# Optimization experiments

Measured on AMD Instinct MI355X. Metric: run time of the kernel, lower is better.

## Reference

```python
import jax, jax.numpy as jnp
import numpy as np
from jax import lax

# init kwargs (hardcoded per module config)
T_D = 0.3            # condensation radius
T_B = 0.85           # min beta threshold
FEATURE_LENGTH = 9   # x[:, FEATURE_LENGTH:] are predictions
N_TOT_FEAT = 17      # => n_ccoords = 17 - 14 = 3
MAX_COND = 1024      # static pad size for the boolean-mask gather output

B = 4
S = 250000
N = B * S


def setup_inputs() -> dict:
    key = jax.random.key(0)
    kx, = jax.random.split(key, 1)
    x = jax.random.uniform(kx, (N, N_TOT_FEAT), dtype=jnp.float32)  # betas in [0,1)
    row_splits = jnp.arange(B + 1, dtype=jnp.int32) * S             # equal ragged splits
    return {"x": x, "row_splits": row_splits}


def _condense(x, n_seg, seg_len):
    """Greedy BuildCondensates (hard/soft=False): per segment, repeatedly pick the
    unassigned point of max beta (>= T_B), assign all unassigned points within
    radius T_D of it in cluster-coordinate space, until no candidate remains."""
    n_ccoords = x.shape[-1] - 14
    x_pred = x[:, FEATURE_LENGTH:]
    betas = x_pred[:, 0].reshape(n_seg, seg_len)                     # (B,S)
    cc = x_pred[:, x_pred.shape[-1] - n_ccoords:].reshape(n_seg, seg_len, n_ccoords)
    col = jnp.arange(seg_len, dtype=jnp.int32)[None, :]              # (1,S)

    asso0 = -jnp.ones((n_seg, seg_len), jnp.int32)
    iscond0 = jnp.zeros((n_seg, seg_len), jnp.int32)

    def body(state):
        asso, iscond, _ = state
        unassigned = asso < 0
        score = jnp.where(unassigned, betas, -jnp.inf)
        max_idx = jnp.argmax(score, axis=1).astype(jnp.int32)        # (B,) per-segment argmax beta
        max_beta = jnp.take_along_axis(score, max_idx[:, None], axis=1)[:, 0]
        found = max_beta >= T_B                                      # (B,)
        c = jnp.take_along_axis(cc, max_idx[:, None, None], axis=1)  # (B,1,nc)
        distsq = jnp.sum((cc - c) ** 2, axis=-1)                     # (B,S)
        assign = unassigned & (distsq < T_D * T_D) & found[:, None]
        asso = jnp.where(assign, max_idx[:, None], asso)
        iscond = jnp.where(assign & (col == max_idx[:, None]), 1, iscond)
        return (asso, iscond, jnp.any(found))

    asso, iscond, _ = lax.while_loop(lambda s: s[2], body,
                                     (asso0, iscond0, jnp.array(True)))
    ncond_per_seg = jnp.sum(iscond, axis=1, dtype=jnp.int32)         # (B,)
    # output row splits for condensates: [0, cumsum...]
    ncond = jnp.concatenate([jnp.zeros((1,), jnp.int32),
                             jnp.cumsum(ncond_per_seg).astype(jnp.int32)])
    return asso, iscond.reshape(-1), ncond


def reference(x, row_splits):
    n_seg = row_splits.shape[0] - 1          # static
    seg_len = x.shape[0] // n_seg            # equal splits assumed (matches setup)
    _, iscond, ncond = _condense(x, n_seg, seg_len)
    # boolean-mask gather dout = x[iscond > 0], padded to static MAX_COND rows
    idx = jnp.nonzero(iscond > 0, size=MAX_COND, fill_value=0)[0]
    total = jnp.sum(iscond)
    valid = (jnp.arange(MAX_COND) < total).astype(x.dtype)           # (K,)
    dout = x[idx] * valid[:, None]                                   # (K, F), zero-padded
    return dout, ncond
```

## Files before the change

kernel.cpp:

```cpp
#include <hip/hip_runtime.h>
#include <stdint.h>

typedef unsigned long long u64;
typedef unsigned int u32;
typedef unsigned char u8;


#define DSQ(ax,ay,az,bx,by,bz) \
    __fadd_rn(__fadd_rn(__fmul_rn(__fsub_rn(ax,bx),__fsub_rn(ax,bx)), \
                        __fmul_rn(__fsub_rn(ay,by),__fsub_rn(ay,by))), \
              __fmul_rn(__fsub_rn(az,bz),__fsub_rn(az,bz)))

#define INS5(k, cx, cy, cz) do { u64 _k = (k); \
    if (_k > K5) { \
      if (_k > K4) { K5 = K4; \
        if (_k > K3) { K4 = K3; X4=X3; Y4=Y3; Z4=Z3; \
          if (_k > K2) { K3 = K2; X3=X2; Y3=Y2; Z3=Z2; \
            if (_k > K1) { K2 = K1; X2=X1; Y2=Y1; Z2=Z1; \
                           K1 = _k; X1=(cx); Y1=(cy); Z1=(cz); } \
            else { K2 = _k; X2=(cx); Y2=(cy); Z2=(cz); } } \
          else { K3 = _k; X3=(cx); Y3=(cy); Z3=(cz); } } \
        else { K4 = _k; X4=(cx); Y4=(cy); Z4=(cz); } } \
      else K5 = _k; \
    } } while (0)

__launch_bounds__(256)
__global__ void filter_scan0(const float* __restrict__ x, int Sg, int chunkG, int bps,
                             int* __restrict__ segCount,
                             float4* __restrict__ A, int* __restrict__ iA,
                             u8* __restrict__ aliveB, int CAP,
                             u64* __restrict__ btK, float4* __restrict__ btC) {
    __shared__ float4 stg[1024];
    __shared__ int sgi[1024];
    __shared__ int s_cnt, s_base;
    __shared__ u64 mK[4][5];
    __shared__ float mC[4][12];
    const int b = blockIdx.x;
    const int s = b / bps, c = b % bps;
    const int tid = threadIdx.x, lane = tid & 63, wid = tid >> 6;
    const int segG0 = s * Sg;
    const int g = segG0 + c * chunkG + tid;
    const bool valid = (g < segG0 + Sg) && (tid < chunkG);
    if (tid == 0) s_cnt = 0;
    __syncthreads();

    float be0=0, be1=0, be2=0, be3=0;
    float4 cc0, cc1, cc2, cc3;
    int r0 = 0;
    if (valid) {
        const float4* p = (const float4*)x + (size_t)g * 17;
        float4 v2 = p[2],  v3 = p[3],  v4 = p[4];
        float4 v6 = p[6],  v7 = p[7],  v8 = p[8];
        float4 v10 = p[10], v12 = p[12];
        float4 v15 = p[15], v16 = p[16];
        r0 = g * 4;
        be0 = v2.y;  cc0 = make_float4(v3.z,  v3.w,  v4.x,  be0);
        be1 = v6.z;  cc1 = make_float4(v7.w,  v8.x,  v8.y,  be1);
        be2 = v10.w; cc2 = make_float4(v12.x, v12.y, v12.z, be2);
        be3 = v15.x; cc3 = make_float4(v16.y, v16.z, v16.w, be3);
    }
    bool h0 = valid && (be0 >= 0.85f), h1 = valid && (be1 >= 0.85f);
    bool h2 = valid && (be2 >= 0.85f), h3 = valid && (be3 >= 0.85f);
    int nh = (h0?1:0) + (h1?1:0) + (h2?1:0) + (h3?1:0);
    int p0 = 0;
    if (nh) p0 = atomicAdd(&s_cnt, nh);
    if (h0) { if (p0 < 1024) { stg[p0] = cc0; sgi[p0] = r0;     } p0++; }
    if (h1) { if (p0 < 1024) { stg[p0] = cc1; sgi[p0] = r0 + 1; } p0++; }
    if (h2) { if (p0 < 1024) { stg[p0] = cc2; sgi[p0] = r0 + 2; } p0++; }
    if (h3) { if (p0 < 1024) { stg[p0] = cc3; sgi[p0] = r0 + 3; } p0++; }
    __syncthreads();
    if (tid == 0) s_base = atomicAdd(&segCount[s], min(s_cnt, 1024));
    __syncthreads();
    int cnt = min(s_cnt, 1024);

    u64 K1=0,K2=0,K3=0,K4=0,K5=0;
    float X1=0,Y1=0,Z1=0,X2=0,Y2=0,Z2=0,X3=0,Y3=0,Z3=0,X4=0,Y4=0,Z4=0;
    for (int k = tid; k < cnt; k += 256) {
        int pos = s_base + k;
        float4 cd = stg[k];
        int gi = sgi[k];
        if (pos < CAP) {
            A[(size_t)s * CAP + pos] = cd;
            iA[(size_t)s * CAP + pos] = gi;
            aliveB[(size_t)s * CAP + pos] = 1;
            u64 key = ((u64)__float_as_uint(cd.w) << 32) | (u64)(~(u32)gi);
            INS5(key, cd.x, cd.y, cd.z);
        }
    }
    for (int off = 32; off > 0; off >>= 1) {
        u64 o1=__shfl_xor(K1,off), o2=__shfl_xor(K2,off), o3=__shfl_xor(K3,off),
            o4=__shfl_xor(K4,off), o5=__shfl_xor(K5,off);
        float a1=__shfl_xor(X1,off), b1=__shfl_xor(Y1,off), c1=__shfl_xor(Z1,off);
        float a2=__shfl_xor(X2,off), b2=__shfl_xor(Y2,off), c2=__shfl_xor(Z2,off);
        float a3=__shfl_xor(X3,off), b3=__shfl_xor(Y3,off), c3=__shfl_xor(Z3,off);
        float a4=__shfl_xor(X4,off), b4=__shfl_xor(Y4,off), c4=__shfl_xor(Z4,off);
        INS5(o1,a1,b1,c1); INS5(o2,a2,b2,c2); INS5(o3,a3,b3,c3); INS5(o4,a4,b4,c4);
        if (o5 > K5) K5 = o5;
    }
    if (lane == 0) {
        mK[wid][0]=K1; mK[wid][1]=K2; mK[wid][2]=K3; mK[wid][3]=K4; mK[wid][4]=K5;
        mC[wid][0]=X1; mC[wid][1]=Y1; mC[wid][2]=Z1; mC[wid][3]=X2; mC[wid][4]=Y2;
        mC[wid][5]=Z2; mC[wid][6]=X3; mC[wid][7]=Y3; mC[wid][8]=Z3; mC[wid][9]=X4;
        mC[wid][10]=Y4; mC[wid][11]=Z4;
    }
    __syncthreads();
    if (tid == 0) {
        for (int w = 1; w < 4; ++w) {
            INS5(mK[w][0], mC[w][0], mC[w][1], mC[w][2]);
            INS5(mK[w][1], mC[w][3], mC[w][4], mC[w][5]);
            INS5(mK[w][2], mC[w][6], mC[w][7], mC[w][8]);
            INS5(mK[w][3], mC[w][9], mC[w][10], mC[w][11]);
            if (mK[w][4] > K5) K5 = mK[w][4];
        }
        btK[(size_t)b*5+0]=K1; btK[(size_t)b*5+1]=K2; btK[(size_t)b*5+2]=K3;
        btK[(size_t)b*5+3]=K4; btK[(size_t)b*5+4]=K5;
        btC[(size_t)b*4+0]=make_float4(X1,Y1,Z1,0.f);
        btC[(size_t)b*4+1]=make_float4(X2,Y2,Z2,0.f);
        btC[(size_t)b*4+2]=make_float4(X3,Y3,Z3,0.f);
        btC[(size_t)b*4+3]=make_float4(X4,Y4,Z4,0.f);
    }
}

__launch_bounds__(256)
__global__ void scan_r(const float4* __restrict__ A, const int* __restrict__ iA,
                       const int* __restrict__ segCount, int CAP,
                       const float4* __restrict__ gctr,
                       const int* __restrict__ condTotal, const int* __restrict__ scanned,
                       const int* __restrict__ doneF, u8* __restrict__ aliveB,
                       u64* __restrict__ btK, float4* __restrict__ btC,
                       int* __restrict__ aliveCnt) {
    const int b = blockIdx.x;
    const int s = b >> 8, c = b & 255;
    const int tid = threadIdx.x, lane = tid & 63, wid = tid >> 6;
    __shared__ float4 ctrL[1024];
    __shared__ u64 mK[4][5];
    __shared__ float mC[4][12];
    __shared__ int wAl[4];
    if (doneF[s]) return;

    int n = segCount[s]; if (n > CAP) n = CAP;
    const int c0 = scanned[s], c1 = condTotal[s];
    const int nc = c1 - c0;
    for (int i = tid; i < nc; i += 256) ctrL[i] = gctr[(size_t)s * 1024 + c0 + i];
    __syncthreads();

    const int chunkC = (n + 255) >> 8;
    const int j0 = c * chunkC;
    const int j1 = min(j0 + chunkC, n);

    u64 K1=0,K2=0,K3=0,K4=0,K5=0;
    float X1=0,Y1=0,Z1=0,X2=0,Y2=0,Z2=0,X3=0,Y3=0,Z3=0,X4=0,Y4=0,Z4=0;
    int myAlive = 0;
    for (int j = j0 + tid; j < j1; j += 256) {
        if (!aliveB[(size_t)s * CAP + j]) continue;
        float4 cd = A[(size_t)s * CAP + j];
        bool live = true;
        for (int m = 0; m < nc; ++m) {
            float4 q = ctrL[m];
            if (DSQ(cd.x, cd.y, cd.z, q.x, q.y, q.z) < 0.09f) { live = false; break; }
        }
        if (!live) { aliveB[(size_t)s * CAP + j] = 0; continue; }
        ++myAlive;
        u64 key = ((u64)__float_as_uint(cd.w) << 32) | (u64)(~(u32)iA[(size_t)s * CAP + j]);
        INS5(key, cd.x, cd.y, cd.z);
    }
    for (int off = 32; off > 0; off >>= 1) {
        u64 o1=__shfl_xor(K1,off), o2=__shfl_xor(K2,off), o3=__shfl_xor(K3,off),
            o4=__shfl_xor(K4,off), o5=__shfl_xor(K5,off);
        float a1=__shfl_xor(X1,off), b1=__shfl_xor(Y1,off), c1v=__shfl_xor(Z1,off);
        float a2=__shfl_xor(X2,off), b2=__shfl_xor(Y2,off), c2v=__shfl_xor(Z2,off);
        float a3=__shfl_xor(X3,off), b3=__shfl_xor(Y3,off), c3v=__shfl_xor(Z3,off);
        float a4=__shfl_xor(X4,off), b4=__shfl_xor(Y4,off), c4v=__shfl_xor(Z4,off);
        INS5(o1,a1,b1,c1v); INS5(o2,a2,b2,c2v); INS5(o3,a3,b3,c3v); INS5(o4,a4,b4,c4v);
        if (o5 > K5) K5 = o5;
        myAlive += __shfl_xor(myAlive, off);
    }
    if (lane == 0) {
        mK[wid][0]=K1; mK[wid][1]=K2; mK[wid][2]=K3; mK[wid][3]=K4; mK[wid][4]=K5;
        mC[wid][0]=X1; mC[wid][1]=Y1; mC[wid][2]=Z1; mC[wid][3]=X2; mC[wid][4]=Y2;
        mC[wid][5]=Z2; mC[wid][6]=X3; mC[wid][7]=Y3; mC[wid][8]=Z3; mC[wid][9]=X4;
        mC[wid][10]=Y4; mC[wid][11]=Z4;
        wAl[wid] = myAlive;
    }
    __syncthreads();
    if (tid == 0) {
        for (int w = 1; w < 4; ++w) {
            INS5(mK[w][0], mC[w][0], mC[w][1], mC[w][2]);
            INS5(mK[w][1], mC[w][3], mC[w][4], mC[w][5]);
            INS5(mK[w][2], mC[w][6], mC[w][7], mC[w][8]);
            INS5(mK[w][3], mC[w][9], mC[w][10], mC[w][11]);
            if (mK[w][4] > K5) K5 = mK[w][4];
        }
        btK[(size_t)b*5+0]=K1; btK[(size_t)b*5+1]=K2; btK[(size_t)b*5+2]=K3;
        btK[(size_t)b*5+3]=K4; btK[(size_t)b*5+4]=K5;
        btC[(size_t)b*4+0]=make_float4(X1,Y1,Z1,0.f);
        btC[(size_t)b*4+1]=make_float4(X2,Y2,Z2,0.f);
        btC[(size_t)b*4+2]=make_float4(X3,Y3,Z3,0.f);
        btC[(size_t)b*4+3]=make_float4(X4,Y4,Z4,0.f);
        int tot = wAl[0] + wAl[1] + wAl[2] + wAl[3];
        if (tot) atomicAdd(&aliveCnt[s], tot);
    }
}

__launch_bounds__(64)
__global__ void pop_k(const u64* __restrict__ btK, const float4* __restrict__ btC,
                      float4* __restrict__ gctr, int* __restrict__ gctrGi,
                      int* __restrict__ condTotal, int* __restrict__ scanned,
                      int* __restrict__ doneF, int* __restrict__ aliveCnt, int check) {
    const int s = blockIdx.x, lane = threadIdx.x;
    if (doneF[s]) return;
    if (check && aliveCnt[s] == 0) { if (lane == 0) doneF[s] = 1; return; }

    u64 k[16]; float4 c[16];
    u64 h = 0;
    #pragma unroll
    for (int q = 0; q < 16; ++q) {
        int bb = (s << 8) + (lane << 2) + (q >> 2);
        int slot = q & 3;
        k[q] = btK[(size_t)bb * 5 + slot];
        c[q] = btC[(size_t)bb * 4 + slot];
        if ((q & 3) == 0) {
            u64 k5 = btK[(size_t)bb * 5 + 4];
            if (k5 > h) h = k5;
        }
    }
    for (int off = 32; off > 0; off >>= 1) {
        u64 o = __shfl_xor(h, off);
        if (o > h) h = o;
    }
    const u64 H = h;

    int ct = condTotal[s];
    const int start = ct;
    while (ct < 1024) {
        u64 mk = k[0]; float4 mc = c[0];
        #pragma unroll
        for (int q = 1; q < 16; ++q)
            if (k[q] > mk) { mk = k[q]; mc = c[q]; }
        int src = lane;
        for (int off = 32; off > 0; off >>= 1) {
            u64 ok = __shfl_xor(mk, off);
            int os = __shfl_xor(src, off);
            if (ok > mk) { mk = ok; src = os; }
        }
        if (mk <= H) break;
        float cx = __shfl(mc.x, src);
        float cy = __shfl(mc.y, src);
        float cz = __shfl(mc.z, src);
        #pragma unroll
        for (int q = 0; q < 16; ++q)
            if (k[q] && DSQ(c[q].x, c[q].y, c[q].z, cx, cy, cz) < 0.09f) k[q] = 0;
        if (lane == 0) {
            gctr[(size_t)s * 1024 + ct] = make_float4(cx, cy, cz, 0.f);
            gctrGi[(size_t)s * 1024 + ct] = (int)(~(u32)(mk & 0xFFFFFFFFull));
        }
        ct++;
    }
    if (lane == 0) { scanned[s] = start; condTotal[s] = ct; aliveCnt[s] = 0; }
}

__launch_bounds__(1024)
__global__ void fallback_k(const float4* __restrict__ A, const int* __restrict__ iA,
                           const int* __restrict__ segCount, int CAP,
                           const float4* __restrict__ gctr, int* __restrict__ gctrGi,
                           int* __restrict__ condTotalG, int* __restrict__ scannedG,
                           const int* __restrict__ doneF, u8* __restrict__ aliveB) {
    const int s = blockIdx.x, tid = threadIdx.x, lane = tid & 63, wid = tid >> 6;
    __shared__ float4 ctr[1024];
    __shared__ int ctrGi[1024];
    __shared__ u64 wk[2][16];
    __shared__ float4 wc[2][16];
    __shared__ u64 s_H;
    __shared__ int s_alive;
    if (doneF[s]) return;

    const float4* cand = A + (size_t)s * CAP;
    const int* gia = iA + (size_t)s * CAP;
    u8* alv = aliveB + (size_t)s * CAP;
    int n = segCount[s]; if (n > CAP) n = CAP;
    int condTotal = condTotalG[s];
    int scanned = scannedG[s];
    for (int i = tid; i < condTotal; i += 1024) {
        ctr[i] = gctr[(size_t)s * 1024 + i];
        ctrGi[i] = gctrGi[(size_t)s * 1024 + i];
    }
    int passes = 0, par = 0;
    __syncthreads();

    while (true) {
        if (tid == 0) { s_H = 0; s_alive = 0; }
        __syncthreads();
        u64 k1 = 0, k2 = 0, k3 = 0;
        float4 C1 = make_float4(0,0,0,0), C2 = make_float4(0,0,0,0);
        int myAlive = 0;
        for (int j = tid; j < n; j += 1024) {
            if (!alv[j]) continue;
            float4 c = cand[j];
            bool live = true;
            for (int m = scanned; m < condTotal; ++m) {
                float4 q = ctr[m];
                if (DSQ(c.x, c.y, c.z, q.x, q.y, q.z) < 0.09f) { live = false; break; }
            }
            if (!live) { alv[j] = 0; continue; }
            ++myAlive;
            u64 key = ((u64)__float_as_uint(c.w) << 32) | (u64)(~(u32)gia[j]);
            if (key > k1)      { k3 = k2; k2 = k1; C2 = C1; k1 = key; C1 = c; }
            else if (key > k2) { k3 = k2; k2 = key; C2 = c; }
            else if (key > k3) { k3 = key; }
        }
        int asum = myAlive; u64 h = k3;
        for (int off = 32; off > 0; off >>= 1) {
            asum += __shfl_down(asum, off);
            u64 o = __shfl_down(h, off);
            if (o > h) h = o;
        }
        if (lane == 0) { atomicAdd(&s_alive, asum); atomicMax(&s_H, h); }
        __syncthreads();
        if (s_alive == 0) break;
        u64 H = s_H;
        scanned = condTotal;
        while (condTotal < 1024) {
            u64 mk; float4 bc;
            if (k1 >= k2) { mk = k1; bc = C1; } else { mk = k2; bc = C2; }
            for (int off = 32; off > 0; off >>= 1) {
                u64 ok = __shfl_xor(mk, off);
                float ox = __shfl_xor(bc.x, off);
                float oy = __shfl_xor(bc.y, off);
                float oz = __shfl_xor(bc.z, off);
                if (ok > mk) { mk = ok; bc.x = ox; bc.y = oy; bc.z = oz; }
            }
            if (lane == 0) { wk[par][wid] = mk; wc[par][wid] = bc; }
            __syncthreads();
            u64 bk = 0; int bL = 0;
            #pragma unroll
            for (int w = 0; w < 16; ++w) {
                u64 kk = wk[par][w];
                if (kk > bk) { bk = kk; bL = w; }
            }
            if (bk <= H) break;
            float4 cc = wc[par][bL];
            if (k1 && DSQ(C1.x, C1.y, C1.z, cc.x, cc.y, cc.z) < 0.09f) k1 = 0;
            if (k2 && DSQ(C2.x, C2.y, C2.z, cc.x, cc.y, cc.z) < 0.09f) k2 = 0;
            if (tid == 0) { ctr[condTotal] = cc; ctrGi[condTotal] = (int)(~(u32)(bk & 0xFFFFFFFFull)); }
            condTotal++;
            par ^= 1;
        }
        __syncthreads();
        if (condTotal >= 1024 || ++passes > 128) break;
    }

    for (int i = tid; i < condTotal; i += 1024)
        gctrGi[(size_t)s * 1024 + i] = ctrGi[i];
    if (tid == 0) condTotalG[s] = condTotal;
}

__global__ void finalize_kernel(const int* __restrict__ ctrGi,
                                const int* __restrict__ condTotal,
                                int* __restrict__ sorted, int* __restrict__ prefix,
                                float* __restrict__ ncond_out, int nseg, int rows) {
    __shared__ int lst[1024];
    __shared__ int pfx[9];
    int tid = threadIdx.x;
    if (tid == 0) {
        int acc = 0; pfx[0] = 0;
        for (int s2 = 0; s2 < nseg; s2++) { acc += condTotal[s2]; pfx[s2 + 1] = acc; }
    }
    __syncthreads();
    if (tid <= nseg) { prefix[tid] = pfx[tid]; ncond_out[tid] = (float)pfx[tid]; }
    for (int s2 = 0; s2 < nseg; s2++) {
        int ns = condTotal[s2]; if (ns > 1024) ns = 1024;
        for (int i = tid; i < ns; i += blockDim.x) lst[i] = ctrGi[(size_t)s2 * 1024 + i];
        __syncthreads();
        for (int i = tid; i < ns; i += blockDim.x) {
            int v = lst[i]; int rank = 0;
            for (int j = 0; j < ns; j++) rank += (lst[j] < v);
            int pos = pfx[s2] + rank;
            if (pos < rows) sorted[pos] = v;
        }
        __syncthreads();
    }
}

__global__ void emit_kernel(const float* __restrict__ x, const int* __restrict__ sorted,
                            const int* __restrict__ prefix, float* __restrict__ out,
                            int rows, int nseg) {
    int e = blockIdx.x * blockDim.x + threadIdx.x;
    if (e >= rows * 17) return;
    int total = prefix[nseg];
    int j = e / 17, k = e - j * 17;
    float v = 0.f;
    if (j < total) v = x[(size_t)sorted[j] * 17 + k];
    out[e] = v;
}

extern "C" void kernel_launch(void* const* d_in, const int* in_sizes, int n_in,
                              void* d_out, int out_size, void* d_ws, size_t ws_size,
                              hipStream_t stream) {
    const float* x = (const float*)d_in[0];
    const int nseg = in_sizes[1] - 1;
    const int N = in_sizes[0] / 17;
    const int S = N / nseg;
    const int rows = (out_size - (nseg + 1)) / 17;
    const int NROUNDS = 2;

    const int bps = 256;
    const int nBlocks = nseg * bps;
    const int Sg = S >> 2;
    const int chunkG = (Sg + bps - 1) / bps;

    size_t fixedBytes = (size_t)nseg * 1024 * 16  +
                        (size_t)nBlocks * 4 * 16  +
                        (size_t)nBlocks * 5 * 8   +
                        (size_t)nseg * 1024 * 4   +
                        (size_t)nseg * 4 * 5  +
                        (size_t)rows * 4 + (size_t)(nseg + 1) * 4 + 8192;
    size_t perCand = (size_t)nseg * (16 + 4 + 1);
    size_t avail = (ws_size > fixedBytes) ? (ws_size - fixedBytes) : 0;
    int CAP = (int)(avail / perCand);
    if (CAP > 65536) CAP = 65536;
    if (CAP < 1) CAP = 1;

    char* w = (char*)d_ws;
    float4* A    = (float4*)w;                 w += (size_t)nseg * CAP * 16;
    float4* ctr  = (float4*)w;                 w += (size_t)nseg * 1024 * 16;
    float4* btC  = (float4*)w;                 w += (size_t)nBlocks * 4 * 16;
    u64* btK     = (u64*)w;                    w += (size_t)nBlocks * 5 * 8;
    int* iA      = (int*)w;                    w += (size_t)nseg * CAP * 4;
    int* ctrGi   = (int*)w;                    w += (size_t)nseg * 1024 * 4;
    int* segCount  = (int*)w;                  w += (size_t)nseg * 4;
    int* condTotal = (int*)w;                  w += (size_t)nseg * 4;
    int* scanned   = (int*)w;                  w += (size_t)nseg * 4;
    int* doneF     = (int*)w;                  w += (size_t)nseg * 4;
    int* aliveCnt  = (int*)w;                  w += (size_t)nseg * 4;
    int* sorted    = (int*)w;                  w += (size_t)rows * 4;
    int* prefix    = (int*)w;                  w += (size_t)(nseg + 1) * 4;
    u8* aliveB     = (u8*)w;
    float* out = (float*)d_out;

    hipMemsetAsync(segCount, 0, (size_t)nseg * 5 * 4, stream);
    filter_scan0<<<nBlocks, 256, 0, stream>>>(x, Sg, chunkG, bps, segCount,
                                              A, iA, aliveB, CAP, btK, btC);
    pop_k<<<nseg, 64, 0, stream>>>(btK, btC, ctr, ctrGi, condTotal, scanned,
                                   doneF, aliveCnt, 0);
    for (int r = 0; r < NROUNDS; ++r) {
        scan_r<<<nBlocks, 256, 0, stream>>>(A, iA, segCount, CAP, ctr, condTotal,
                                            scanned, doneF, aliveB, btK, btC, aliveCnt);
        pop_k<<<nseg, 64, 0, stream>>>(btK, btC, ctr, ctrGi, condTotal, scanned,
                                       doneF, aliveCnt, 1);
    }
    fallback_k<<<nseg, 1024, 0, stream>>>(A, iA, segCount, CAP, ctr, ctrGi,
                                          condTotal, scanned, doneF, aliveB);
    finalize_kernel<<<1, 256, 0, stream>>>(ctrGi, condTotal, sorted, prefix,
                                           out + (size_t)rows * 17, nseg, rows);
    emit_kernel<<<(rows * 17 + 255) / 256, 256, 0, stream>>>(x, sorted, prefix, out,
                                                             rows, nseg);
}
```

Measured before the change: 158.0 us.

## Drop scan rounds, go straight to fallback, fuse finalize and emit

```diff
diff --git a/kernel.cpp b/kernel.cpp
--- a/kernel.cpp
+++ b/kernel.cpp
@@ -121,104 +121,22 @@
     }
 }
 
-__launch_bounds__(256)
-__global__ void scan_r(const float4* __restrict__ A, const int* __restrict__ iA,
-                       const int* __restrict__ segCount, int CAP,
-                       const float4* __restrict__ gctr,
-                       const int* __restrict__ condTotal, const int* __restrict__ scanned,
-                       const int* __restrict__ doneF, u8* __restrict__ aliveB,
-                       u64* __restrict__ btK, float4* __restrict__ btC,
-                       int* __restrict__ aliveCnt) {
-    const int b = blockIdx.x;
-    const int s = b >> 8, c = b & 255;
-    const int tid = threadIdx.x, lane = tid & 63, wid = tid >> 6;
-    __shared__ float4 ctrL[1024];
-    __shared__ u64 mK[4][5];
-    __shared__ float mC[4][12];
-    __shared__ int wAl[4];
-    if (doneF[s]) return;
-
-    int n = segCount[s]; if (n > CAP) n = CAP;
-    const int c0 = scanned[s], c1 = condTotal[s];
-    const int nc = c1 - c0;
-    for (int i = tid; i < nc; i += 256) ctrL[i] = gctr[(size_t)s * 1024 + c0 + i];
-    __syncthreads();
-
-    const int chunkC = (n + 255) >> 8;
-    const int j0 = c * chunkC;
-    const int j1 = min(j0 + chunkC, n);
-
-    u64 K1=0,K2=0,K3=0,K4=0,K5=0;
-    float X1=0,Y1=0,Z1=0,X2=0,Y2=0,Z2=0,X3=0,Y3=0,Z3=0,X4=0,Y4=0,Z4=0;
-    int myAlive = 0;
-    for (int j = j0 + tid; j < j1; j += 256) {
-        if (!aliveB[(size_t)s * CAP + j]) continue;
-        float4 cd = A[(size_t)s * CAP + j];
-        bool live = true;
-        for (int m = 0; m < nc; ++m) {
-            float4 q = ctrL[m];
-            if (DSQ(cd.x, cd.y, cd.z, q.x, q.y, q.z) < 0.09f) { live = false; break; }
-        }
-        if (!live) { aliveB[(size_t)s * CAP + j] = 0; continue; }
-        ++myAlive;
-        u64 key = ((u64)__float_as_uint(cd.w) << 32) | (u64)(~(u32)iA[(size_t)s * CAP + j]);
-        INS5(key, cd.x, cd.y, cd.z);
-    }
-    for (int off = 32; off > 0; off >>= 1) {
-        u64 o1=__shfl_xor(K1,off), o2=__shfl_xor(K2,off), o3=__shfl_xor(K3,off),
-            o4=__shfl_xor(K4,off), o5=__shfl_xor(K5,off);
-        float a1=__shfl_xor(X1,off), b1=__shfl_xor(Y1,off), c1v=__shfl_xor(Z1,off);
-        float a2=__shfl_xor(X2,off), b2=__shfl_xor(Y2,off), c2v=__shfl_xor(Z2,off);
-        float a3=__shfl_xor(X3,off), b3=__shfl_xor(Y3,off), c3v=__shfl_xor(Z3,off);
-        float a4=__shfl_xor(X4,off), b4=__shfl_xor(Y4,off), c4v=__shfl_xor(Z4,off);
-        INS5(o1,a1,b1,c1v); INS5(o2,a2,b2,c2v); INS5(o3,a3,b3,c3v); INS5(o4,a4,b4,c4v);
-        if (o5 > K5) K5 = o5;
-        myAlive += __shfl_xor(myAlive, off);
-    }
-    if (lane == 0) {
-        mK[wid][0]=K1; mK[wid][1]=K2; mK[wid][2]=K3; mK[wid][3]=K4; mK[wid][4]=K5;
-        mC[wid][0]=X1; mC[wid][1]=Y1; mC[wid][2]=Z1; mC[wid][3]=X2; mC[wid][4]=Y2;
-        mC[wid][5]=Z2; mC[wid][6]=X3; mC[wid][7]=Y3; mC[wid][8]=Z3; mC[wid][9]=X4;
-        mC[wid][10]=Y4; mC[wid][11]=Z4;
-        wAl[wid] = myAlive;
-    }
-    __syncthreads();
-    if (tid == 0) {
-        for (int w = 1; w < 4; ++w) {
-            INS5(mK[w][0], mC[w][0], mC[w][1], mC[w][2]);
-            INS5(mK[w][1], mC[w][3], mC[w][4], mC[w][5]);
-            INS5(mK[w][2], mC[w][6], mC[w][7], mC[w][8]);
-            INS5(mK[w][3], mC[w][9], mC[w][10], mC[w][11]);
-            if (mK[w][4] > K5) K5 = mK[w][4];
-        }
-        btK[(size_t)b*5+0]=K1; btK[(size_t)b*5+1]=K2; btK[(size_t)b*5+2]=K3;
-        btK[(size_t)b*5+3]=K4; btK[(size_t)b*5+4]=K5;
-        btC[(size_t)b*4+0]=make_float4(X1,Y1,Z1,0.f);
-        btC[(size_t)b*4+1]=make_float4(X2,Y2,Z2,0.f);
-        btC[(size_t)b*4+2]=make_float4(X3,Y3,Z3,0.f);
-        btC[(size_t)b*4+3]=make_float4(X4,Y4,Z4,0.f);
-        int tot = wAl[0] + wAl[1] + wAl[2] + wAl[3];
-        if (tot) atomicAdd(&aliveCnt[s], tot);
-    }
-}
-
 __launch_bounds__(64)
 __global__ void pop_k(const u64* __restrict__ btK, const float4* __restrict__ btC,
                       float4* __restrict__ gctr, int* __restrict__ gctrGi,
                       int* __restrict__ condTotal, int* __restrict__ scanned,
-                      int* __restrict__ doneF, int* __restrict__ aliveCnt, int check) {
+                      int* __restrict__ doneF, int* __restrict__ aliveCnt) {
     const int s = blockIdx.x, lane = threadIdx.x;
-    if (doneF[s]) return;
-    if (check && aliveCnt[s] == 0) { if (lane == 0) doneF[s] = 1; return; }
-
-    u64 k[16]; float4 c[16];
+
+    u64 k[16]; float cx16[16], cy16[16], cz16[16];
     u64 h = 0;
     #pragma unroll
     for (int q = 0; q < 16; ++q) {
         int bb = (s << 8) + (lane << 2) + (q >> 2);
         int slot = q & 3;
         k[q] = btK[(size_t)bb * 5 + slot];
-        c[q] = btC[(size_t)bb * 4 + slot];
+        float4 t = btC[(size_t)bb * 4 + slot];
+        cx16[q] = t.x; cy16[q] = t.y; cz16[q] = t.z;
         if ((q & 3) == 0) {
             u64 k5 = btK[(size_t)bb * 5 + 4];
             if (k5 > h) h = k5;
@@ -233,10 +151,10 @@
     int ct = condTotal[s];
     const int start = ct;
     while (ct < 1024) {
-        u64 mk = k[0]; float4 mc = c[0];
+        u64 mk = k[0]; float mx = cx16[0], my = cy16[0], mz = cz16[0];
         #pragma unroll
         for (int q = 1; q < 16; ++q)
-            if (k[q] > mk) { mk = k[q]; mc = c[q]; }
+            if (k[q] > mk) { mk = k[q]; mx = cx16[q]; my = cy16[q]; mz = cz16[q]; }
         int src = lane;
         for (int off = 32; off > 0; off >>= 1) {
             u64 ok = __shfl_xor(mk, off);
@@ -244,19 +162,19 @@
             if (ok > mk) { mk = ok; src = os; }
         }
         if (mk <= H) break;
-        float cx = __shfl(mc.x, src);
-        float cy = __shfl(mc.y, src);
-        float cz = __shfl(mc.z, src);
+        float cx = __shfl(mx, src);
+        float cy = __shfl(my, src);
+        float cz = __shfl(mz, src);
         #pragma unroll
         for (int q = 0; q < 16; ++q)
-            if (k[q] && DSQ(c[q].x, c[q].y, c[q].z, cx, cy, cz) < 0.09f) k[q] = 0;
+            if (k[q] && DSQ(cx16[q], cy16[q], cz16[q], cx, cy, cz) < 0.09f) k[q] = 0;
         if (lane == 0) {
             gctr[(size_t)s * 1024 + ct] = make_float4(cx, cy, cz, 0.f);
             gctrGi[(size_t)s * 1024 + ct] = (int)(~(u32)(mk & 0xFFFFFFFFull));
         }
         ct++;
     }
-    if (lane == 0) { scanned[s] = start; condTotal[s] = ct; aliveCnt[s] = 0; }
+    if (lane == 0) { scanned[s] = start; condTotal[s] = ct; }
 }
 
 __launch_bounds__(1024)
@@ -264,7 +182,7 @@
                            const int* __restrict__ segCount, int CAP,
                            const float4* __restrict__ gctr, int* __restrict__ gctrGi,
                            int* __restrict__ condTotalG, int* __restrict__ scannedG,
-                           const int* __restrict__ doneF, u8* __restrict__ aliveB) {
+                           u8* __restrict__ aliveB) {
     const int s = blockIdx.x, tid = threadIdx.x, lane = tid & 63, wid = tid >> 6;
     __shared__ float4 ctr[1024];
     __shared__ int ctrGi[1024];
@@ -272,7 +190,6 @@
     __shared__ float4 wc[2][16];
     __shared__ u64 s_H;
     __shared__ int s_alive;
-    if (doneF[s]) return;
 
     const float4* cand = A + (size_t)s * CAP;
     const int* gia = iA + (size_t)s * CAP;
@@ -354,11 +271,13 @@
     if (tid == 0) condTotalG[s] = condTotal;
 }
 
-__global__ void finalize_kernel(const int* __restrict__ ctrGi,
-                                const int* __restrict__ condTotal,
-                                int* __restrict__ sorted, int* __restrict__ prefix,
-                                float* __restrict__ ncond_out, int nseg, int rows) {
+__launch_bounds__(1024)
+__global__ void finalize_emit(const float* __restrict__ x,
+                              const int* __restrict__ ctrGi,
+                              const int* __restrict__ condTotal,
+                              float* __restrict__ out, int rows, int nseg) {
     __shared__ int lst[1024];
+    __shared__ int srt[1024];
     __shared__ int pfx[9];
     int tid = threadIdx.x;
     if (tid == 0) {
@@ -366,31 +285,27 @@
         for (int s2 = 0; s2 < nseg; s2++) { acc += condTotal[s2]; pfx[s2 + 1] = acc; }
     }
     __syncthreads();
-    if (tid <= nseg) { prefix[tid] = pfx[tid]; ncond_out[tid] = (float)pfx[tid]; }
+    float* ncond_out = out + (size_t)rows * 17;
+    if (tid <= nseg) ncond_out[tid] = (float)pfx[tid];
     for (int s2 = 0; s2 < nseg; s2++) {
         int ns = condTotal[s2]; if (ns > 1024) ns = 1024;
-        for (int i = tid; i < ns; i += blockDim.x) lst[i] = ctrGi[(size_t)s2 * 1024 + i];
-        __syncthreads();
-        for (int i = tid; i < ns; i += blockDim.x) {
+        for (int i = tid; i < ns; i += 1024) lst[i] = ctrGi[(size_t)s2 * 1024 + i];
+        __syncthreads();
+        for (int i = tid; i < ns; i += 1024) {
             int v = lst[i]; int rank = 0;
             for (int j = 0; j < ns; j++) rank += (lst[j] < v);
             int pos = pfx[s2] + rank;
-            if (pos < rows) sorted[pos] = v;
-        }
-        __syncthreads();
-    }
-}
-
-__global__ void emit_kernel(const float* __restrict__ x, const int* __restrict__ sorted,
-                            const int* __restrict__ prefix, float* __restrict__ out,
-                            int rows, int nseg) {
-    int e = blockIdx.x * blockDim.x + threadIdx.x;
-    if (e >= rows * 17) return;
-    int total = prefix[nseg];
-    int j = e / 17, k = e - j * 17;
-    float v = 0.f;
-    if (j < total) v = x[(size_t)sorted[j] * 17 + k];
-    out[e] = v;
+            if (pos < rows) srt[pos] = v;
+        }
+        __syncthreads();
+    }
+    int total = pfx[nseg];
+    for (int e = tid; e < rows * 17; e += 1024) {
+        int j = e / 17, kk = e - j * 17;
+        float v = 0.f;
+        if (j < total) v = x[(size_t)srt[j] * 17 + kk];
+        out[e] = v;
+    }
 }
 
 extern "C" void kernel_launch(void* const* d_in, const int* in_sizes, int n_in,
@@ -401,7 +316,6 @@
     const int N = in_sizes[0] / 17;
     const int S = N / nseg;
     const int rows = (out_size - (nseg + 1)) / 17;
-    const int NROUNDS = 2;
 
     const int bps = 256;
     const int nBlocks = nseg * bps;
@@ -412,8 +326,7 @@
                         (size_t)nBlocks * 4 * 16  +
                         (size_t)nBlocks * 5 * 8   +
                         (size_t)nseg * 1024 * 4   +
-                        (size_t)nseg * 4 * 5  +
-                        (size_t)rows * 4 + (size_t)(nseg + 1) * 4 + 8192;
+                        (size_t)nseg * 4 * 5  + 8192;
     size_t perCand = (size_t)nseg * (16 + 4 + 1);
     size_t avail = (ws_size > fixedBytes) ? (ws_size - fixedBytes) : 0;
     int CAP = (int)(avail / perCand);
@@ -432,8 +345,6 @@
     int* scanned   = (int*)w;                  w += (size_t)nseg * 4;
     int* doneF     = (int*)w;                  w += (size_t)nseg * 4;
     int* aliveCnt  = (int*)w;                  w += (size_t)nseg * 4;
-    int* sorted    = (int*)w;                  w += (size_t)rows * 4;
-    int* prefix    = (int*)w;                  w += (size_t)(nseg + 1) * 4;
     u8* aliveB     = (u8*)w;
     float* out = (float*)d_out;
 
@@ -441,17 +352,8 @@
     filter_scan0<<<nBlocks, 256, 0, stream>>>(x, Sg, chunkG, bps, segCount,
                                               A, iA, aliveB, CAP, btK, btC);
     pop_k<<<nseg, 64, 0, stream>>>(btK, btC, ctr, ctrGi, condTotal, scanned,
-                                   doneF, aliveCnt, 0);
-    for (int r = 0; r < NROUNDS; ++r) {
-        scan_r<<<nBlocks, 256, 0, stream>>>(A, iA, segCount, CAP, ctr, condTotal,
-                                            scanned, doneF, aliveB, btK, btC, aliveCnt);
-        pop_k<<<nseg, 64, 0, stream>>>(btK, btC, ctr, ctrGi, condTotal, scanned,
-                                       doneF, aliveCnt, 1);
-    }
+                                   doneF, aliveCnt);
     fallback_k<<<nseg, 1024, 0, stream>>>(A, iA, segCount, CAP, ctr, ctrGi,
-                                          condTotal, scanned, doneF, aliveB);
-    finalize_kernel<<<1, 256, 0, stream>>>(ctrGi, condTotal, sorted, prefix,
-                                           out + (size_t)rows * 17, nseg, rows);
-    emit_kernel<<<(rows * 17 + 255) / 256, 256, 0, stream>>>(x, sorted, prefix, out,
-                                                             rows, nseg);
-}
+                                          condTotal, scanned, aliveB);
+    finalize_emit<<<1, 1024, 0, stream>>>(x, ctrGi, condTotal, out, rows, nseg);
+}
```

Result: slower. 367.6 us (+132.7%).
